# Kernel optimization log

Measured on AMD Instinct MI355X. Metric: run time of the kernel, lower is better.

The kernel has to match this reference:

```python
import jax, jax.numpy as jnp
import numpy as np

IN_FEATS = 512
OUT_FEATS = 512
N = 8192
M = 8192


def setup_inputs() -> dict:
    key = jax.random.key(0)
    k1, k2, k3 = jax.random.split(key, 3)
    feat_p = jax.random.normal(k1, (N, IN_FEATS), dtype=jnp.float32)
    feat_s = jax.random.normal(k2, (M, IN_FEATS), dtype=jnp.float32)
    # He (kaiming uniform) init: bound = sqrt(6 / fan_in)
    bound = float(np.sqrt(6.0 / IN_FEATS))
    weight_a = jax.random.uniform(k3, (IN_FEATS, OUT_FEATS), dtype=jnp.float32,
                                  minval=-bound, maxval=bound)
    return {"feat_p": feat_p, "feat_s": feat_s, "weight_a": weight_a}


def reference(feat_p, feat_s, weight_a):
    h_i = feat_p @ weight_a            # [N, out]
    h_j = feat_s @ weight_a            # [M, out]
    a_ij = jax.nn.relu(h_i @ h_j.T)    # [N, M]
    fro = jnp.sqrt(jnp.sum(a_ij * a_ij))
    alpha = a_ij / fro                 # global Frobenius-norm normalization
    c_i = alpha @ feat_s               # [N, in]
    return c_i
```

## Files before the change

kernel.cpp:

```cpp
#include <hip/hip_runtime.h>
#include <hip/hip_bf16.h>

#define NROWS 8192
#define DIM   512

typedef short v8s __attribute__((ext_vector_type(8)));
typedef float v4f __attribute__((ext_vector_type(4)));

#define ASM_VMCNT(n) asm volatile("s_waitcnt vmcnt(" #n ")" ::: "memory")
#define ASM_LGKM0    asm volatile("s_waitcnt lgkmcnt(0)" ::: "memory")
#define ASM_FENCE    asm volatile("" ::: "memory")
#define BAR          __builtin_amdgcn_s_barrier()

__device__ __forceinline__ short f2bf(float f) {
    union { float f; unsigned u; } v; v.f = f;
    unsigned r = (v.u + 0x7fffu + ((v.u >> 16) & 1u)) >> 16;
    return (short)r;
}

__device__ __forceinline__ void stage16(const void* g, void* l) {
    typedef __attribute__((address_space(1))) const unsigned GA;
    typedef __attribute__((address_space(3))) unsigned LA;
    __builtin_amdgcn_global_load_lds((GA*)(const unsigned*)g, (LA*)(unsigned*)l, 16, 0, 0);
}

__global__ __launch_bounds__(256) void transpose_cast_kernel(
        const float* __restrict__ in, short* __restrict__ out, int R, int C) {
    __shared__ float t[32][33];
    const int lx = threadIdx.x & 31;
    const int ly = threadIdx.x >> 5;
    const int r0 = blockIdx.x * 32;
    const int c0 = blockIdx.y * 32;
#pragma unroll
    for (int p = 0; p < 4; ++p)
        t[ly + 8 * p][lx] = in[(size_t)(r0 + ly + 8 * p) * C + c0 + lx];
    __syncthreads();
#pragma unroll
    for (int p = 0; p < 4; ++p)
        out[(size_t)(c0 + ly + 8 * p) * R + r0 + lx] = f2bf(t[lx][ly + 8 * p]);
}

__global__ __launch_bounds__(256) void gemm1_kernel(
        const float* __restrict__ Fp, const float* __restrict__ Fs,
        const short* __restrict__ WT,
        short* __restrict__ Hp, short* __restrict__ Hs) {
    const float* F = blockIdx.z ? Fs : Fp;
    short* H = blockIdx.z ? Hs : Hp;
    const int lane = threadIdx.x & 63;
    const int wid  = threadIdx.x >> 6;
    const int lr = lane & 15, lg = lane >> 4;
    const int r0 = blockIdx.x * 64 + wid * 16;
    const int c0 = blockIdx.y * 64;

    v4f acc[4] = {};
#pragma unroll
    for (int kc = 0; kc < 16; ++kc) {
        const int k = kc * 32 + lg * 8;
        const float* ap = F + (size_t)(r0 + lr) * DIM + k;
        float4 f0 = *(const float4*)ap;
        float4 f1 = *(const float4*)(ap + 4);
        v8s a;
        a[0] = f2bf(f0.x); a[1] = f2bf(f0.y); a[2] = f2bf(f0.z); a[3] = f2bf(f0.w);
        a[4] = f2bf(f1.x); a[5] = f2bf(f1.y); a[6] = f2bf(f1.z); a[7] = f2bf(f1.w);
#pragma unroll
        for (int ct = 0; ct < 4; ++ct) {
            v8s b = *(const v8s*)(WT + (size_t)(c0 + ct * 16 + lr) * DIM + k);
            acc[ct] = __builtin_amdgcn_mfma_f32_16x16x32_bf16(a, b, acc[ct], 0, 0, 0);
        }
    }
#pragma unroll
    for (int ct = 0; ct < 4; ++ct)
#pragma unroll
        for (int i = 0; i < 4; ++i)
            H[(size_t)(r0 + lg * 4 + i) * DIM + c0 + ct * 16 + lr] = f2bf(acc[ct][i]);
}

#define JSPLIT 2
#define JT_PER_BLOCK (NROWS / 64 / JSPLIT)

__device__ __forceinline__ void stage_full(const char* __restrict__ HsB,
        char* ringW, int j0, int tid) {
#pragma unroll
    for (int s = 0; s < 8; ++s) {
        const int L = s * 8192 + tid * 16;
        const int row = L >> 10;
        const int c = (L & 1023) ^ ((row & 7) << 4);
        stage16(HsB + ((size_t)(j0 + row) << 10) + c, ringW + L);
    }
}

__device__ __forceinline__ void phase_b(const short (*SbR)[72], const v8s* bF,
        v4f (&accC)[16], int lr, int lg) {
    __builtin_amdgcn_s_setprio(1);
#pragma unroll
    for (int kc2 = 0; kc2 < 2; ++kc2)
#pragma unroll
        for (int mt = 0; mt < 4; ++mt) {
            v8s aS = *(const v8s*)&SbR[mt * 16 + lr][kc2 * 32 + lg * 8];
#pragma unroll
            for (int ct = 0; ct < 4; ++ct)
                accC[mt * 4 + ct] = __builtin_amdgcn_mfma_f32_16x16x32_bf16(
                    aS, bF[ct * 2 + kc2], accC[mt * 4 + ct], 0, 0, 0);
        }
    __builtin_amdgcn_s_setprio(0);
}

__global__ __launch_bounds__(512, 2) void fused_kernel(
        const short* __restrict__ Hp, const short* __restrict__ Hs,
        const short* __restrict__ FsT, float* __restrict__ Cacc,
        float* __restrict__ ssq) {
    __shared__ __align__(16) short HsL[2][64][512];
    __shared__ __align__(16) short Sb[2][64][72];

    const int tid  = threadIdx.x;
    const int lane = tid & 63;
    const int wid  = tid >> 6;
    const int lr = lane & 15, lg = lane >> 4;
    const int strip = wid >> 1;
    const int half  = wid & 1;

    const int nwg = gridDim.x * gridDim.y;
    const int bid = blockIdx.x + gridDim.x * blockIdx.y;
    const int cpx = nwg >> 3;
    const int swz = (bid & 7) * cpx + (bid >> 3);
    const int bx = swz % gridDim.x;
    const int by = swz / gridDim.x;

    const int m0  = bx * 64;
    const int jt0 = by * JT_PER_BLOCK;

    v8s afrag[16];
#pragma unroll
    for (int kk = 0; kk < 16; ++kk)
        afrag[kk] = *(const v8s*)(Hp +
            (size_t)(m0 + strip * 16 + lr) * DIM + kk * 32 + lg * 8);

    v4f accC[16] = {};
    float ssq_l = 0.f;

    stage_full((const char*)Hs, (char*)&HsL[0][0][0], jt0 * 64, tid);
    ASM_VMCNT(0);

    const int xo = (lr & 7) << 4;

    for (int t = 0; t < JT_PER_BLOCK; ++t) {
        const int jcur  = (jt0 + t) * 64;
        const int jnext = (t + 1 < JT_PER_BLOCK) ? jcur + 64 : jt0 * 64;
        const char* ringR = (const char*)&HsL[t & 1][0][0];
        char*       ringW = (char*)&HsL[(t + 1) & 1][0][0];

        BAR;
        ASM_FENCE;

        v8s bF[8];
        if (t > 0) {
            const int jprev = jcur - 64;
#pragma unroll
            for (int ct = 0; ct < 4; ++ct)
#pragma unroll
                for (int kc2 = 0; kc2 < 2; ++kc2)
                    bF[ct * 2 + kc2] = *(const v8s*)(FsT +
                        (size_t)(wid * 64 + ct * 16 + lr) * NROWS + jprev + kc2 * 32 + lg * 8);
        }
        ASM_FENCE;
        stage_full((const char*)Hs, ringW, jnext, tid);

        v4f s0 = {}, s1 = {};
        {
            const char* rp0 = ringR + (size_t)(half * 32 + lr) * 1024;
            const char* rp1 = rp0 + 16 * 1024;
            __builtin_amdgcn_s_setprio(1);
#pragma unroll
            for (int kk = 0; kk < 16; ++kk) {
                const int off = (kk * 64 + lg * 16) ^ xo;
                v8s hb0 = *(const v8s*)(rp0 + off);
                v8s hb1 = *(const v8s*)(rp1 + off);
                s0 = __builtin_amdgcn_mfma_f32_16x16x32_bf16(afrag[kk], hb0, s0, 0, 0, 0);
                s1 = __builtin_amdgcn_mfma_f32_16x16x32_bf16(afrag[kk], hb1, s1, 0, 0, 0);
            }
            __builtin_amdgcn_s_setprio(0);
        }

        if (t > 0) {
            ASM_VMCNT(8);
            phase_b(Sb[(t - 1) & 1], bF, accC, lr, lg);
        }

        short (*SbW)[72] = Sb[t & 1];
#pragma unroll
        for (int i = 0; i < 4; ++i) {
            float v0 = fmaxf(s0[i], 0.f), v1 = fmaxf(s1[i], 0.f);
            ssq_l += v0 * v0 + v1 * v1;
            const int r = strip * 16 + lg * 4 + i;
            SbW[r][(half * 2 + 0) * 16 + lr] = f2bf(v0);
            SbW[r][(half * 2 + 1) * 16 + lr] = f2bf(v1);
        }
        ASM_LGKM0;
        ASM_VMCNT(0);
    }

    BAR;
    {
        const int jprev = (jt0 + JT_PER_BLOCK - 1) * 64;
        v8s bF[8];
#pragma unroll
        for (int ct = 0; ct < 4; ++ct)
#pragma unroll
            for (int kc2 = 0; kc2 < 2; ++kc2)
                bF[ct * 2 + kc2] = *(const v8s*)(FsT +
                    (size_t)(wid * 64 + ct * 16 + lr) * NROWS + jprev + kc2 * 32 + lg * 8);
        ASM_VMCNT(0);
        phase_b(Sb[(JT_PER_BLOCK - 1) & 1], bF, accC, lr, lg);
    }

    float w = ssq_l;
#pragma unroll
    for (int off = 32; off; off >>= 1) w += __shfl_down(w, off);
    if (lane == 0) atomicAdd(ssq, w);

#pragma unroll
    for (int mt = 0; mt < 4; ++mt)
#pragma unroll
        for (int ct = 0; ct < 4; ++ct)
#pragma unroll
            for (int i = 0; i < 4; ++i)
                atomicAdd(&Cacc[(size_t)(m0 + mt * 16 + lg * 4 + i) * DIM +
                                wid * 64 + ct * 16 + lr],
                          accC[mt * 4 + ct][i]);
}

__global__ __launch_bounds__(256) void scale_kernel(float* __restrict__ C,
                                                    const float* __restrict__ ssq) {
    const float rs = 1.0f / sqrtf(*ssq);
    const size_t i = (size_t)blockIdx.x * blockDim.x + threadIdx.x;
    float4* p = (float4*)C;
    float4 v = p[i];
    v.x *= rs; v.y *= rs; v.z *= rs; v.w *= rs;
    p[i] = v;
}

extern "C" void kernel_launch(void* const* d_in, const int* in_sizes, int n_in,
                              void* d_out, int out_size, void* d_ws, size_t ws_size,
                              hipStream_t stream) {
    const float* feat_p   = (const float*)d_in[0];
    const float* feat_s   = (const float*)d_in[1];
    const float* weight_a = (const float*)d_in[2];

    char* ws = (char*)d_ws;
    float* ssqp = (float*)ws;
    short* WT   = (short*)(ws + 512);
    short* Hp   = (short*)(ws + 512 + 524288);
    short* Hs   = (short*)(ws + 512 + 524288 + 8388608);
    short* FsT  = (short*)(ws + 512 + 524288 + 16777216);

    transpose_cast_kernel<<<dim3(DIM / 32, DIM / 32), 256, 0, stream>>>(weight_a, WT, DIM, DIM);
    transpose_cast_kernel<<<dim3(NROWS / 32, DIM / 32), 256, 0, stream>>>(feat_s, FsT, NROWS, DIM);

    gemm1_kernel<<<dim3(NROWS / 64, DIM / 64, 2), 256, 0, stream>>>(
        feat_p, feat_s, WT, Hp, Hs);

    hipMemsetAsync(d_out, 0, (size_t)out_size * sizeof(float), stream);
    hipMemsetAsync(ssqp, 0, sizeof(float), stream);

    fused_kernel<<<dim3(NROWS / 64, JSPLIT), 512, 0, stream>>>(Hp, Hs, FsT, (float*)d_out, ssqp);

    scale_kernel<<<(out_size / 4 + 255) / 256, 256, 0, stream>>>((float*)d_out, ssqp);
}
```

Baseline: 385.2 us.

## Retile first GEMM for A-fragment reuse and prefetch FsT one iteration early

The first projection GEMM now converts each wave's 16-row slice of the fp32 features to bf16 once into registers. It then loops over 256 output columns, rather than re-reading and re-converting the input for every 64-column tile, using 512-thread blocks. In the fused kernel, the per-iteration FsT fragment loads move to the end of the previous iteration so their latency overlaps the next barrier and score MFMAs, and phase_b moves after the ReLU/store step. This raises register pressure (the A fragments are held across the column loop) and changes the vmcnt wait accounting, which could stall or misorder waits.

```diff
diff --git a/kernel.cpp b/kernel.cpp
--- a/kernel.cpp
+++ b/kernel.cpp
@@ -40,7 +40,7 @@
         out[(size_t)(c0 + ly + 8 * p) * R + r0 + lx] = f2bf(t[lx][ly + 8 * p]);
 }
 
-__global__ __launch_bounds__(256) void gemm1_kernel(
+__global__ __launch_bounds__(512) void gemm1_kernel(
         const float* __restrict__ Fp, const float* __restrict__ Fs,
         const short* __restrict__ WT,
         short* __restrict__ Hp, short* __restrict__ Hs) {
@@ -49,30 +49,37 @@
     const int lane = threadIdx.x & 63;
     const int wid  = threadIdx.x >> 6;
     const int lr = lane & 15, lg = lane >> 4;
-    const int r0 = blockIdx.x * 64 + wid * 16;
-    const int c0 = blockIdx.y * 64;
-
-    v4f acc[4] = {};
-#pragma unroll
-    for (int kc = 0; kc < 16; ++kc) {
-        const int k = kc * 32 + lg * 8;
-        const float* ap = F + (size_t)(r0 + lr) * DIM + k;
+    const int r0 = blockIdx.x * 128 + wid * 16;
+    const int c0 = blockIdx.y * 256;
+
+    v8s a[16];
+#pragma unroll
+    for (int kk = 0; kk < 16; ++kk) {
+        const float* ap = F + (size_t)(r0 + lr) * DIM + kk * 32 + lg * 8;
         float4 f0 = *(const float4*)ap;
         float4 f1 = *(const float4*)(ap + 4);
-        v8s a;
-        a[0] = f2bf(f0.x); a[1] = f2bf(f0.y); a[2] = f2bf(f0.z); a[3] = f2bf(f0.w);
-        a[4] = f2bf(f1.x); a[5] = f2bf(f1.y); a[6] = f2bf(f1.z); a[7] = f2bf(f1.w);
-#pragma unroll
-        for (int ct = 0; ct < 4; ++ct) {
-            v8s b = *(const v8s*)(WT + (size_t)(c0 + ct * 16 + lr) * DIM + k);
-            acc[ct] = __builtin_amdgcn_mfma_f32_16x16x32_bf16(a, b, acc[ct], 0, 0, 0);
-        }
-    }
-#pragma unroll
-    for (int ct = 0; ct < 4; ++ct)
-#pragma unroll
-        for (int i = 0; i < 4; ++i)
-            H[(size_t)(r0 + lg * 4 + i) * DIM + c0 + ct * 16 + lr] = f2bf(acc[ct][i]);
+        v8s t;
+        t[0] = f2bf(f0.x); t[1] = f2bf(f0.y); t[2] = f2bf(f0.z); t[3] = f2bf(f0.w);
+        t[4] = f2bf(f1.x); t[5] = f2bf(f1.y); t[6] = f2bf(f1.z); t[7] = f2bf(f1.w);
+        a[kk] = t;
+    }
+
+    for (int ctp = 0; ctp < 8; ++ctp) {
+        const int cb = c0 + ctp * 32;
+        v4f acc0 = {}, acc1 = {};
+#pragma unroll
+        for (int kk = 0; kk < 16; ++kk) {
+            v8s b0 = *(const v8s*)(WT + (size_t)(cb + lr) * DIM + kk * 32 + lg * 8);
+            v8s b1 = *(const v8s*)(WT + (size_t)(cb + 16 + lr) * DIM + kk * 32 + lg * 8);
+            acc0 = __builtin_amdgcn_mfma_f32_16x16x32_bf16(a[kk], b0, acc0, 0, 0, 0);
+            acc1 = __builtin_amdgcn_mfma_f32_16x16x32_bf16(a[kk], b1, acc1, 0, 0, 0);
+        }
+#pragma unroll
+        for (int i = 0; i < 4; ++i) {
+            H[(size_t)(r0 + lg * 4 + i) * DIM + cb + lr]      = f2bf(acc0[i]);
+            H[(size_t)(r0 + lg * 4 + i) * DIM + cb + 16 + lr] = f2bf(acc1[i]);
+        }
+    }
 }
 
 #define JSPLIT 2
@@ -136,6 +143,7 @@
             (size_t)(m0 + strip * 16 + lr) * DIM + kk * 32 + lg * 8);
 
     v4f accC[16] = {};
+    v8s bF[8];
     float ssq_l = 0.f;
 
     stage_full((const char*)Hs, (char*)&HsL[0][0][0], jt0 * 64, tid);
@@ -152,17 +160,6 @@
         BAR;
         ASM_FENCE;
 
-        v8s bF[8];
-        if (t > 0) {
-            const int jprev = jcur - 64;
-#pragma unroll
-            for (int ct = 0; ct < 4; ++ct)
-#pragma unroll
-                for (int kc2 = 0; kc2 < 2; ++kc2)
-                    bF[ct * 2 + kc2] = *(const v8s*)(FsT +
-                        (size_t)(wid * 64 + ct * 16 + lr) * NROWS + jprev + kc2 * 32 + lg * 8);
-        }
-        ASM_FENCE;
         stage_full((const char*)Hs, ringW, jnext, tid);
 
         v4f s0 = {}, s1 = {};
@@ -181,11 +178,6 @@
             __builtin_amdgcn_s_setprio(0);
         }
 
-        if (t > 0) {
-            ASM_VMCNT(8);
-            phase_b(Sb[(t - 1) & 1], bF, accC, lr, lg);
-        }
-
         short (*SbW)[72] = Sb[t & 1];
 #pragma unroll
         for (int i = 0; i < 4; ++i) {
@@ -195,23 +187,26 @@
             SbW[r][(half * 2 + 0) * 16 + lr] = f2bf(v0);
             SbW[r][(half * 2 + 1) * 16 + lr] = f2bf(v1);
         }
+
+        if (t > 0) {
+            ASM_VMCNT(8);
+            phase_b(Sb[(t - 1) & 1], bF, accC, lr, lg);
+        }
         ASM_LGKM0;
-        ASM_VMCNT(0);
-    }
-
-    BAR;
-    {
-        const int jprev = (jt0 + JT_PER_BLOCK - 1) * 64;
-        v8s bF[8];
+
+        ASM_FENCE;
 #pragma unroll
         for (int ct = 0; ct < 4; ++ct)
 #pragma unroll
             for (int kc2 = 0; kc2 < 2; ++kc2)
                 bF[ct * 2 + kc2] = *(const v8s*)(FsT +
-                    (size_t)(wid * 64 + ct * 16 + lr) * NROWS + jprev + kc2 * 32 + lg * 8);
-        ASM_VMCNT(0);
-        phase_b(Sb[(JT_PER_BLOCK - 1) & 1], bF, accC, lr, lg);
-    }
+                    (size_t)(wid * 64 + ct * 16 + lr) * NROWS + jcur + kc2 * 32 + lg * 8);
+        ASM_VMCNT(8);
+    }
+
+    BAR;
+    ASM_VMCNT(0);
+    phase_b(Sb[(JT_PER_BLOCK - 1) & 1], bF, accC, lr, lg);
 
     float w = ssq_l;
 #pragma unroll
@@ -256,7 +251,7 @@
     transpose_cast_kernel<<<dim3(DIM / 32, DIM / 32), 256, 0, stream>>>(weight_a, WT, DIM, DIM);
     transpose_cast_kernel<<<dim3(NROWS / 32, DIM / 32), 256, 0, stream>>>(feat_s, FsT, NROWS, DIM);
 
-    gemm1_kernel<<<dim3(NROWS / 64, DIM / 64, 2), 256, 0, stream>>>(
+    gemm1_kernel<<<dim3(NROWS / 128, 2, 2), 512, 0, stream>>>(
         feat_p, feat_s, WT, Hp, Hs);
 
     hipMemsetAsync(d_out, 0, (size_t)out_size * sizeof(float), stream);
```

Measured after the change: 353.0 us. 1.09x faster.
